# Kernel optimization log

Hardware: AMD Instinct MI355X
Metric: run time of the kernel (lower is better)

Reference implementation:

```python
import jax, jax.numpy as jnp
import numpy as np

N = 8192      # nodes; also input feature dim (x.shape[0] used as in_channels)
E = 524288    # edges per edge type (avg degree 64)
H = 200       # hidden dim (hard-coded in RecomNet)
MEAN_RATING = 3.5


def setup_inputs() -> dict:
    key = jax.random.key(0)
    ks = jax.random.split(key, 14)
    s_in = np.float32(1.0 / np.sqrt(N))
    s_h = np.float32(1.0 / np.sqrt(H))
    return {
        "x": jax.random.normal(ks[0], (N, N), jnp.float32),
        "edge_sim": jax.random.randint(ks[1], (2, E), 0, N),
        "edge_rat": jax.random.randint(ks[2], (2, E), 0, N),
        "mask": jax.random.randint(ks[3], (E,), 0, 2).astype(bool),
        # conv1 params (in=N, out=H)
        "w1_self": jax.random.normal(ks[4], (N, H), jnp.float32) * s_in,
        "w1_sim": jax.random.normal(ks[5], (N, H), jnp.float32) * s_in,
        "w1_rat": jax.random.normal(ks[6], (N, H), jnp.float32) * s_in,
        "b1": jnp.zeros((H,), jnp.float32),
        # conv2 params (in=H, out=H)
        "w2_self": jax.random.normal(ks[7], (H, H), jnp.float32) * s_h,
        "w2_sim": jax.random.normal(ks[8], (H, H), jnp.float32) * s_h,
        "w2_rat": jax.random.normal(ks[9], (H, H), jnp.float32) * s_h,
        "b2": jnp.zeros((H,), jnp.float32),
        # bilinear decoder
        "Q": jax.random.normal(ks[10], (H, H), jnp.float32) * s_h,
    }


def _recom_conv(edge_sim, edge_rat, x, w_self, w_sim, w_rat, b):
    # linear-then-gather-then-scatter (linear commutes with sum aggregation)
    m_sim = (x @ w_sim)[edge_sim[0]]                                   # [E, H]
    agg_sim = jax.ops.segment_sum(m_sim, edge_sim[1], num_segments=N)  # [N, H]
    m_rat = (x @ w_rat)[edge_rat[0]]
    agg_rat = jax.ops.segment_sum(m_rat, edge_rat[1], num_segments=N)
    return x @ w_self + agg_sim + agg_rat + b


def reference(x, w1_self, w1_sim, w1_rat, b1, w2_self, w2_sim, w2_rat, b2, Q,
              edge_sim, edge_rat, mask):
    h = _recom_conv(edge_sim, edge_rat, x, w1_self, w1_sim, w1_rat, b1)
    h = jax.nn.relu(h)
    h = _recom_conv(edge_sim, edge_rat, h, w2_self, w2_sim, w2_rat, b2)
    h1 = h[edge_rat[0]]                                                # [E, H]
    h2 = h[edge_rat[1]]                                                # [E, H]
    pred = jnp.einsum("eh,hk,ek->e", h1, Q, h2) + MEAN_RATING          # [E]
    # original compacts with boolean mask (dynamic shape); here we keep a
    # fixed [E] output and zero out unmasked edges
    return jnp.where(mask, pred, 0.0)
```

## Files before the change

kernel.cpp:

```cpp
#include <hip/hip_runtime.h>

#define NN 8192
#define EE 524288
#define HPAD 256
#define NP 640

using s16x8 = __attribute__((ext_vector_type(8))) short;
using f32x4 = __attribute__((ext_vector_type(4))) float;

__device__ __forceinline__ unsigned short f2b(float f) {
    unsigned u = __float_as_uint(f);
    u = (u + 0x7FFFu + ((u >> 16) & 1u)) >> 16;
    return (unsigned short)u;
}
__device__ __forceinline__ float b2f(unsigned short u) {
    return __uint_as_float((unsigned)u << 16);
}

__device__ __forceinline__ void async16(const unsigned short* g, unsigned short* l)
{
    __builtin_amdgcn_global_load_lds(
        (const __attribute__((address_space(1))) unsigned int*)g,
        (__attribute__((address_space(3))) unsigned int*)l, 16, 0, 0);
}


__global__ void cvt_f2b_kernel(const float* __restrict__ in,
                               unsigned short* __restrict__ out, int n4)
{
    int i = blockIdx.x * 256 + threadIdx.x;
    if (i >= n4) return;
    float4 v = ((const float4*)in)[i];
    ushort4 o;
    o.x = f2b(v.x); o.y = f2b(v.y); o.z = f2b(v.z); o.w = f2b(v.w);
    ((ushort4*)out)[i] = o;
}

__global__ void transpose_w_kernel(const float* __restrict__ w0,
                                   const float* __restrict__ w1,
                                   const float* __restrict__ w2,
                                   unsigned short* __restrict__ out,
                                   int Kout, int Kreal, int Nreal)
{
    __shared__ float tile[32][33];
    const int kb = blockIdx.x << 5;
    const int nb = blockIdx.y << 5;
    const int tx = threadIdx.x, ty = threadIdx.y;
    const int n = nb + tx;
    const float* w = (n < 200) ? w0 : (n < 400) ? w1 : w2;
    const int c = (n < 200) ? n : (n < 400) ? n - 200 : n - 400;
#pragma unroll
    for (int i = 0; i < 4; ++i) {
        const int k = kb + ty + (i << 3);
        float v = 0.f;
        if (n < Nreal && k < Kreal) v = w[(size_t)k * 200 + c];
        tile[ty + (i << 3)][tx] = v;
    }
    __syncthreads();
#pragma unroll
    for (int i = 0; i < 4; ++i) {
        const int nn = nb + ty + (i << 3);
        out[(size_t)nn * Kout + kb + tx] = f2b(tile[tx][ty + (i << 3)]);
    }
}

__global__ __launch_bounds__(256) void gemm_mfma(
    const unsigned short* __restrict__ A,
    const unsigned short* __restrict__ BT,
    float* __restrict__ C, unsigned short* __restrict__ Cb,
    int lda, int KC, int ldc, size_t planeStride)
{
    __shared__ unsigned short As[2][128 * 64];
    __shared__ unsigned short Bs[2][128 * 64];
    const int tid  = threadIdx.x;
    const int lane = tid & 63;
    const int w    = tid >> 6;

    const int nx   = gridDim.x;
    const int flat = blockIdx.y * nx + blockIdx.x;
    const int cpx  = (nx * gridDim.y) >> 3;
    const int orig = (flat & 7) * cpx + (flat >> 3);
    const int by   = orig / nx;
    const int bx   = orig - by * nx;

    const int row0 = by << 7;
    const int col0 = bx << 7;
    const int z    = blockIdx.z;
    const int wm = (w >> 1) << 6;
    const int wn = (w & 1) << 6;

    const int sr = lane >> 3;
    const int sc = (lane & 7) ^ sr;
    const size_t kbase = (size_t)z * KC + ((size_t)sc << 3);
    const unsigned short* aG = A  + (size_t)(row0 + w * 8 + sr) * lda + kbase;
    const unsigned short* bG = BT + (size_t)(col0 + w * 8 + sr) * lda + kbase;
    const int ldsOff = w * 8;

    const f32x4 zero = {0.f, 0.f, 0.f, 0.f};
    f32x4 acc[4][4];
#pragma unroll
    for (int i = 0; i < 4; ++i)
#pragma unroll
        for (int j = 0; j < 4; ++j) acc[i][j] = zero;

#pragma unroll
    for (int it = 0; it < 4; ++it) {
        async16(aG + (size_t)(it * 32) * lda, &As[0][(it * 32 + ldsOff) << 6]);
        async16(bG + (size_t)(it * 32) * lda, &Bs[0][(it * 32 + ldsOff) << 6]);
    }
    __syncthreads();

    const int T = KC >> 6;
    for (int t = 0; t < T; ++t) {
        const int cur = t & 1;
        if (t + 1 < T) {
            const int ko = (t + 1) << 6;
#pragma unroll
            for (int it = 0; it < 4; ++it) {
                async16(aG + (size_t)(it * 32) * lda + ko,
                        &As[cur ^ 1][(it * 32 + ldsOff) << 6]);
                async16(bG + (size_t)(it * 32) * lda + ko,
                        &Bs[cur ^ 1][(it * 32 + ldsOff) << 6]);
            }
        }
#pragma unroll
        for (int kk = 0; kk < 2; ++kk) {
            const int q  = (kk << 2) + (lane >> 4);
            const int sl = (q ^ (lane & 7)) << 3;
            s16x8 af[4], bfv[4];
#pragma unroll
            for (int i = 0; i < 4; ++i) {
                const int rm = wm + (i << 4) + (lane & 15);
                af[i]  = *(const s16x8*)(&As[cur][(rm << 6) + sl]);
                const int rn = wn + (i << 4) + (lane & 15);
                bfv[i] = *(const s16x8*)(&Bs[cur][(rn << 6) + sl]);
            }
#pragma unroll
            for (int i = 0; i < 4; ++i)
#pragma unroll
                for (int j = 0; j < 4; ++j)
                    acc[i][j] = __builtin_amdgcn_mfma_f32_16x16x32_bf16(
                        af[i], bfv[j], acc[i][j], 0, 0, 0);
        }
        __syncthreads();
    }

    const int cr = (lane >> 4) << 2;
    const int cc = lane & 15;
    if (Cb) {
#pragma unroll
        for (int i = 0; i < 4; ++i)
#pragma unroll
            for (int j = 0; j < 4; ++j)
#pragma unroll
                for (int r = 0; r < 4; ++r)
                    Cb[(size_t)(row0 + wm + (i << 4) + cr + r) * ldc
                       + (col0 + wn + (j << 4) + cc)] = f2b(acc[i][j][r]);
    } else {
        float* Cp = C + (size_t)z * planeStride;
#pragma unroll
        for (int i = 0; i < 4; ++i)
#pragma unroll
            for (int j = 0; j < 4; ++j)
#pragma unroll
                for (int r = 0; r < 4; ++r)
                    Cp[(size_t)(row0 + wm + (i << 4) + cr + r) * ldc
                       + (col0 + wn + (j << 4) + cc)] = acc[i][j][r];
    }
}

__global__ void combine_kernel(const float* __restrict__ p0,
                               const float* __restrict__ p1,
                               float* __restrict__ y_self,
                               unsigned short* __restrict__ y_simb,
                               unsigned short* __restrict__ y_ratb)
{
    int t = blockIdx.x * 256 + threadIdx.x;
    int n = t / 50, j4 = (t - n * 50) << 2;
    const float* a = p0 + (size_t)n * NP;
    float4 s = *(const float4*)(a + j4);
    float4 m = *(const float4*)(a + 200 + j4);
    float4 r = *(const float4*)(a + 400 + j4);
    if (p1) {
        const float* b = p1 + (size_t)n * NP;
        float4 s2 = *(const float4*)(b + j4);
        float4 m2 = *(const float4*)(b + 200 + j4);
        float4 r2 = *(const float4*)(b + 400 + j4);
        s.x += s2.x; s.y += s2.y; s.z += s2.z; s.w += s2.w;
        m.x += m2.x; m.y += m2.y; m.z += m2.z; m.w += m2.w;
        r.x += r2.x; r.y += r2.y; r.z += r2.z; r.w += r2.w;
    }
    *(float4*)(y_self + (size_t)n * 200 + j4) = s;
    ushort4 mo, ro;
    mo.x = f2b(m.x); mo.y = f2b(m.y); mo.z = f2b(m.z); mo.w = f2b(m.w);
    ro.x = f2b(r.x); ro.y = f2b(r.y); ro.z = f2b(r.z); ro.w = f2b(r.w);
    *(ushort4*)(y_simb + (size_t)n * 200 + j4) = mo;
    *(ushort4*)(y_ratb + (size_t)n * 200 + j4) = ro;
}


__global__ void hist_kernel(const int* __restrict__ e0, const int* __restrict__ e1,
                            int* __restrict__ d0, int* __restrict__ d1)
{
    const int* edges = blockIdx.y ? e1 : e0;
    int* deg = blockIdx.y ? d1 : d0;
    int e = blockIdx.x * 256 + threadIdx.x;
    if (e < EE) atomicAdd(&deg[edges[EE + e]], 1);
}

__global__ void scan_kernel(const int* __restrict__ deg0, int* __restrict__ off0,
                            int* __restrict__ pos0,
                            const int* __restrict__ deg1, int* __restrict__ off1,
                            int* __restrict__ pos1)
{
    const int* deg = blockIdx.x ? deg1 : deg0;
    int* off = blockIdx.x ? off1 : off0;
    int* pos = blockIdx.x ? pos1 : pos0;
    __shared__ int part[256];
    const int t = threadIdx.x;
    const int base = t * 32;
    int s = 0;
#pragma unroll
    for (int i = 0; i < 32; ++i) s += deg[base + i];
    part[t] = s;
    __syncthreads();
    for (int d = 1; d < 256; d <<= 1) {
        int v = (t >= d) ? part[t - d] : 0;
        __syncthreads();
        part[t] += v;
        __syncthreads();
    }
    int run = (t == 0) ? 0 : part[t - 1];
    for (int i = 0; i < 32; ++i) {
        off[base + i] = run;
        pos[base + i] = run;
        run += deg[base + i];
    }
    if (t == 255) off[NN] = run;
}

__global__ void reorder_kernel(const int* __restrict__ e0, int* __restrict__ pos0,
                               int2* __restrict__ se0,
                               const int* __restrict__ e1, int* __restrict__ pos1,
                               int2* __restrict__ se1)
{
    const int* edges = blockIdx.y ? e1 : e0;
    int* pos = blockIdx.y ? pos1 : pos0;
    int2* se = blockIdx.y ? se1 : se0;
    int e = blockIdx.x * 256 + threadIdx.x;
    if (e >= EE) return;
    int p = atomicAdd(&pos[edges[EE + e]], 1);
    se[p] = make_int2(edges[e], e);
}


__device__ __forceinline__ void edge_accum(
    const unsigned short* __restrict__ msg,
    const int* __restrict__ off, const int2* __restrict__ se,
    int n, int w, int j4, bool act, float4& acc)
{
    const int e1 = off[n + 1];
    int i = off[n] + w;
    for (; i + 12 < e1; i += 16) {
        const int s0 = se[i].x;
        const int s1 = se[i + 4].x;
        const int s2 = se[i + 8].x;
        const int s3 = se[i + 12].x;
        if (act) {
            ushort4 v0 = *(const ushort4*)(msg + (size_t)s0 * 200 + j4);
            ushort4 v1 = *(const ushort4*)(msg + (size_t)s1 * 200 + j4);
            ushort4 v2 = *(const ushort4*)(msg + (size_t)s2 * 200 + j4);
            ushort4 v3 = *(const ushort4*)(msg + (size_t)s3 * 200 + j4);
            acc.x += (b2f(v0.x) + b2f(v1.x)) + (b2f(v2.x) + b2f(v3.x));
            acc.y += (b2f(v0.y) + b2f(v1.y)) + (b2f(v2.y) + b2f(v3.y));
            acc.z += (b2f(v0.z) + b2f(v1.z)) + (b2f(v2.z) + b2f(v3.z));
            acc.w += (b2f(v0.w) + b2f(v1.w)) + (b2f(v2.w) + b2f(v3.w));
        }
    }
    for (; i < e1; i += 4) {
        const int s = se[i].x;
        if (act) {
            ushort4 v = *(const ushort4*)(msg + (size_t)s * 200 + j4);
            acc.x += b2f(v.x); acc.y += b2f(v.y);
            acc.z += b2f(v.z); acc.w += b2f(v.w);
        }
    }
}

__global__ __launch_bounds__(256) void agg_fused_kernel(
    const unsigned short* __restrict__ msg_sim,
    const unsigned short* __restrict__ msg_rat,
    const int* __restrict__ off_sim, const int2* __restrict__ se_sim,
    const int* __restrict__ off_rat, const int2* __restrict__ se_rat,
    const float* __restrict__ y_self, const float* __restrict__ bias,
    unsigned short* __restrict__ hb, int relu)
{
    __shared__ float part[4][200];
    const int n = blockIdx.x;
    const int w = threadIdx.x >> 6;
    const int lane = threadIdx.x & 63;
    const int j4 = lane << 2;
    const bool act = lane < 50;

    float4 acc = {0.f, 0.f, 0.f, 0.f};
    edge_accum(msg_sim, off_sim, se_sim, n, w, j4, act, acc);
    edge_accum(msg_rat, off_rat, se_rat, n, w, j4, act, acc);

    if (act) *(float4*)&part[w][j4] = acc;
    __syncthreads();
    const int j = threadIdx.x;
    if (j < 200) {
        float v = part[0][j] + part[1][j] + part[2][j] + part[3][j]
                + y_self[(size_t)n * 200 + j] + bias[j];
        if (relu) v = fmaxf(v, 0.f);
        hb[((size_t)n << 8) + j] = f2b(v);
    } else if (j < HPAD) {
        hb[((size_t)n << 8) + j] = 0;
    }
}

__global__ __launch_bounds__(256) void pred_kernel(
    const unsigned short* __restrict__ hQb,
    const unsigned short* __restrict__ h2b,
    const int* __restrict__ off, const int2* __restrict__ se,
    const int* __restrict__ mask, float* __restrict__ out)
{
    const int n = blockIdx.x;
    const int w = threadIdx.x >> 6;
    const int lane = threadIdx.x & 63;
    float4 b = {0.f, 0.f, 0.f, 0.f};
    if (lane < 50) {
        ushort4 v = *(const ushort4*)(h2b + ((size_t)n << 8) + (lane << 2));
        b.x = b2f(v.x); b.y = b2f(v.y); b.z = b2f(v.z); b.w = b2f(v.w);
    }
    const int e1 = off[n + 1];
    int i = off[n] + w;
    for (; i + 12 < e1; i += 16) {
        const int2 p0 = se[i];
        const int2 p1 = se[i + 4];
        const int2 p2 = se[i + 8];
        const int2 p3 = se[i + 12];
        float s0 = 0.f, s1 = 0.f, s2 = 0.f, s3 = 0.f;
        if (lane < 50) {
            ushort4 a0 = *(const ushort4*)(hQb + ((size_t)p0.x << 8) + (lane << 2));
            ushort4 a1 = *(const ushort4*)(hQb + ((size_t)p1.x << 8) + (lane << 2));
            ushort4 a2 = *(const ushort4*)(hQb + ((size_t)p2.x << 8) + (lane << 2));
            ushort4 a3 = *(const ushort4*)(hQb + ((size_t)p3.x << 8) + (lane << 2));
            s0 = fmaf(b2f(a0.x), b.x, fmaf(b2f(a0.y), b.y,
                 fmaf(b2f(a0.z), b.z, b2f(a0.w) * b.w)));
            s1 = fmaf(b2f(a1.x), b.x, fmaf(b2f(a1.y), b.y,
                 fmaf(b2f(a1.z), b.z, b2f(a1.w) * b.w)));
            s2 = fmaf(b2f(a2.x), b.x, fmaf(b2f(a2.y), b.y,
                 fmaf(b2f(a2.z), b.z, b2f(a2.w) * b.w)));
            s3 = fmaf(b2f(a3.x), b.x, fmaf(b2f(a3.y), b.y,
                 fmaf(b2f(a3.z), b.z, b2f(a3.w) * b.w)));
        }
#pragma unroll
        for (int o = 32; o > 0; o >>= 1) {
            s0 += __shfl_down(s0, o, 64);
            s1 += __shfl_down(s1, o, 64);
            s2 += __shfl_down(s2, o, 64);
            s3 += __shfl_down(s3, o, 64);
        }
        if (lane == 0) {
            out[p0.y] = mask[p0.y] ? (s0 + 3.5f) : 0.f;
            out[p1.y] = mask[p1.y] ? (s1 + 3.5f) : 0.f;
            out[p2.y] = mask[p2.y] ? (s2 + 3.5f) : 0.f;
            out[p3.y] = mask[p3.y] ? (s3 + 3.5f) : 0.f;
        }
    }
    for (; i < e1; i += 4) {
        const int2 p = se[i];
        float s = 0.f;
        if (lane < 50) {
            ushort4 a = *(const ushort4*)(hQb + ((size_t)p.x << 8) + (lane << 2));
            s = fmaf(b2f(a.x), b.x, fmaf(b2f(a.y), b.y,
                fmaf(b2f(a.z), b.z, b2f(a.w) * b.w)));
        }
#pragma unroll
        for (int o = 32; o > 0; o >>= 1) s += __shfl_down(s, o, 64);
        if (lane == 0) out[p.y] = mask[p.y] ? (s + 3.5f) : 0.f;
    }
}

extern "C" void kernel_launch(void* const* d_in, const int* in_sizes, int n_in,
                              void* d_out, int out_size, void* d_ws, size_t ws_size,
                              hipStream_t stream)
{
    const float* x       = (const float*)d_in[0];
    const int*   e_sim   = (const int*)d_in[1];
    const int*   e_rat   = (const int*)d_in[2];
    const int*   mask    = (const int*)d_in[3];
    const float* w1_self = (const float*)d_in[4];
    const float* w1_sim  = (const float*)d_in[5];
    const float* w1_rat  = (const float*)d_in[6];
    const float* b1      = (const float*)d_in[7];
    const float* w2_self = (const float*)d_in[8];
    const float* w2_sim  = (const float*)d_in[9];
    const float* w2_rat  = (const float*)d_in[10];
    const float* b2      = (const float*)d_in[11];
    const float* Q       = (const float*)d_in[12];
    float* out = (float*)d_out;

    char* p = (char*)d_ws;
    auto alloc = [&](size_t bytes) -> char* {
        char* r = p;
        p += (bytes + 255) & ~(size_t)255;
        return r;
    };
    unsigned short* xb    = (unsigned short*)alloc((size_t)NN * NN * 2);
    unsigned short* wbT1  = (unsigned short*)alloc((size_t)NP * NN * 2);
    unsigned short* wbT2  = (unsigned short*)alloc((size_t)NP * HPAD * 2);
    unsigned short* QT    = (unsigned short*)alloc((size_t)HPAD * HPAD * 2);
    float* ypart = (float*)alloc((size_t)2 * NN * NP * 4);
    float* y_self = (float*)alloc((size_t)NN * 200 * 4);
    unsigned short* y_simb = (unsigned short*)alloc((size_t)NN * 200 * 2);
    unsigned short* y_ratb = (unsigned short*)alloc((size_t)NN * 200 * 2);
    unsigned short* h1b = (unsigned short*)alloc((size_t)NN * HPAD * 2);
    unsigned short* h2b = (unsigned short*)alloc((size_t)NN * HPAD * 2);
    unsigned short* hQb = (unsigned short*)alloc((size_t)NN * HPAD * 2);
    int* deg_sim = (int*)alloc(NN * 4);
    int* deg_rat = (int*)alloc(NN * 4);
    int* off_sim = (int*)alloc((NN + 1) * 4);
    int* off_rat = (int*)alloc((NN + 1) * 4);
    int* pos_sim = (int*)alloc(NN * 4);
    int* pos_rat = (int*)alloc(NN * 4);
    int2* se_sim = (int2*)alloc((size_t)EE * 8);
    int2* se_rat = (int2*)alloc((size_t)EE * 8);

    const dim3 blk(256);
    const dim3 tblk(32, 8);

    cvt_f2b_kernel<<<(NN * NN / 4) / 256, blk, 0, stream>>>(x, xb, NN * NN / 4);
    transpose_w_kernel<<<dim3(NN / 32, NP / 32), tblk, 0, stream>>>(
        w1_self, w1_sim, w1_rat, wbT1, NN, NN, 600);
    transpose_w_kernel<<<dim3(HPAD / 32, NP / 32), tblk, 0, stream>>>(
        w2_self, w2_sim, w2_rat, wbT2, HPAD, 200, 600);
    transpose_w_kernel<<<dim3(HPAD / 32, HPAD / 32), tblk, 0, stream>>>(
        Q, Q, Q, QT, HPAD, 200, 200);

    hipMemsetAsync(deg_sim, 0, 2 * NN * 4, stream);
    hist_kernel<<<dim3(EE / 256, 2), blk, 0, stream>>>(e_sim, e_rat, deg_sim, deg_rat);
    scan_kernel<<<2, blk, 0, stream>>>(deg_sim, off_sim, pos_sim,
                                       deg_rat, off_rat, pos_rat);
    reorder_kernel<<<dim3(EE / 256, 2), blk, 0, stream>>>(
        e_sim, pos_sim, se_sim, e_rat, pos_rat, se_rat);

    gemm_mfma<<<dim3(NP / 128, NN / 128, 2), blk, 0, stream>>>(
        xb, wbT1, ypart, nullptr, NN, NN / 2, NP, (size_t)NN * NP);
    combine_kernel<<<NN * 50 / 256, blk, 0, stream>>>(
        ypart, ypart + (size_t)NN * NP, y_self, y_simb, y_ratb);
    agg_fused_kernel<<<NN, blk, 0, stream>>>(
        y_simb, y_ratb, off_sim, se_sim, off_rat, se_rat, y_self, b1, h1b, 1);

    gemm_mfma<<<dim3(NP / 128, NN / 128, 1), blk, 0, stream>>>(
        h1b, wbT2, ypart, nullptr, HPAD, HPAD, NP, 0);
    combine_kernel<<<NN * 50 / 256, blk, 0, stream>>>(
        ypart, nullptr, y_self, y_simb, y_ratb);
    agg_fused_kernel<<<NN, blk, 0, stream>>>(
        y_simb, y_ratb, off_sim, se_sim, off_rat, se_rat, y_self, b2, h2b, 0);

    gemm_mfma<<<dim3(HPAD / 128, NN / 128, 1), blk, 0, stream>>>(
        h2b, QT, nullptr, hQb, HPAD, HPAD, HPAD, 0);
    pred_kernel<<<NN, blk, 0, stream>>>(hQb, h2b, off_rat, se_rat, mask, out);
}
```

Measured before the change: 850.0 us.

## Raise layer-1 split-K to four planes and fuse layer-2 combine into GEMM epilogue

The big layer-1 GEMM (8192x640x8192) now uses split-K of 4 instead of 2, giving 1280 blocks instead of 640 so the GPU's compute units are better occupied. The combine kernel is generalized to sum an arbitrary number of partial planes. For layer 2, the GEMM epilogue now writes y_self as fp32 and y_sim/y_rat as bf16 directly, removing the intermediate fp32 buffer and one kernel launch. The cost is twice the partial-sum traffic for layer 1 and branchy, scattered epilogue stores.

```diff
diff --git a/kernel.cpp b/kernel.cpp
--- a/kernel.cpp
+++ b/kernel.cpp
@@ -68,7 +68,9 @@
     const unsigned short* __restrict__ A,
     const unsigned short* __restrict__ BT,
     float* __restrict__ C, unsigned short* __restrict__ Cb,
-    int lda, int KC, int ldc, size_t planeStride)
+    int lda, int KC, int ldc, size_t planeStride,
+    float* __restrict__ ys, unsigned short* __restrict__ ysb,
+    unsigned short* __restrict__ yrb)
 {
     __shared__ unsigned short As[2][128 * 64];
     __shared__ unsigned short Bs[2][128 * 64];
@@ -147,7 +149,21 @@
 
     const int cr = (lane >> 4) << 2;
     const int cc = lane & 15;
-    if (Cb) {
+    if (ysb) {
+#pragma unroll
+        for (int i = 0; i < 4; ++i)
+#pragma unroll
+            for (int j = 0; j < 4; ++j)
+#pragma unroll
+                for (int r = 0; r < 4; ++r) {
+                    const int n = row0 + wm + (i << 4) + cr + r;
+                    const int c = col0 + wn + (j << 4) + cc;
+                    const float v = acc[i][j][r];
+                    if (c < 200)      ys [(size_t)n * 200 + c]        = v;
+                    else if (c < 400) ysb[(size_t)n * 200 + (c - 200)] = f2b(v);
+                    else if (c < 600) yrb[(size_t)n * 200 + (c - 400)] = f2b(v);
+                }
+    } else if (Cb) {
 #pragma unroll
         for (int i = 0; i < 4; ++i)
 #pragma unroll
@@ -169,23 +185,21 @@
     }
 }
 
-__global__ void combine_kernel(const float* __restrict__ p0,
-                               const float* __restrict__ p1,
+__global__ void combine_kernel(const float* __restrict__ parts, int nplanes,
                                float* __restrict__ y_self,
                                unsigned short* __restrict__ y_simb,
                                unsigned short* __restrict__ y_ratb)
 {
     int t = blockIdx.x * 256 + threadIdx.x;
     int n = t / 50, j4 = (t - n * 50) << 2;
-    const float* a = p0 + (size_t)n * NP;
-    float4 s = *(const float4*)(a + j4);
-    float4 m = *(const float4*)(a + 200 + j4);
-    float4 r = *(const float4*)(a + 400 + j4);
-    if (p1) {
-        const float* b = p1 + (size_t)n * NP;
-        float4 s2 = *(const float4*)(b + j4);
-        float4 m2 = *(const float4*)(b + 200 + j4);
-        float4 r2 = *(const float4*)(b + 400 + j4);
+    float4 s = {0.f, 0.f, 0.f, 0.f};
+    float4 m = {0.f, 0.f, 0.f, 0.f};
+    float4 r = {0.f, 0.f, 0.f, 0.f};
+    for (int z = 0; z < nplanes; ++z) {
+        const float* a = parts + (size_t)z * NN * NP + (size_t)n * NP;
+        float4 s2 = *(const float4*)(a + j4);
+        float4 m2 = *(const float4*)(a + 200 + j4);
+        float4 r2 = *(const float4*)(a + 400 + j4);
         s.x += s2.x; s.y += s2.y; s.z += s2.z; s.w += s2.w;
         m.x += m2.x; m.y += m2.y; m.z += m2.z; m.w += m2.w;
         r.x += r2.x; r.y += r2.y; r.z += r2.z; r.w += r2.w;
@@ -412,7 +426,7 @@
     unsigned short* wbT1  = (unsigned short*)alloc((size_t)NP * NN * 2);
     unsigned short* wbT2  = (unsigned short*)alloc((size_t)NP * HPAD * 2);
     unsigned short* QT    = (unsigned short*)alloc((size_t)HPAD * HPAD * 2);
-    float* ypart = (float*)alloc((size_t)2 * NN * NP * 4);
+    float* ypart = (float*)alloc((size_t)4 * NN * NP * 4);
     float* y_self = (float*)alloc((size_t)NN * 200 * 4);
     unsigned short* y_simb = (unsigned short*)alloc((size_t)NN * 200 * 2);
     unsigned short* y_ratb = (unsigned short*)alloc((size_t)NN * 200 * 2);
@@ -446,21 +460,22 @@
     reorder_kernel<<<dim3(EE / 256, 2), blk, 0, stream>>>(
         e_sim, pos_sim, se_sim, e_rat, pos_rat, se_rat);
 
-    gemm_mfma<<<dim3(NP / 128, NN / 128, 2), blk, 0, stream>>>(
-        xb, wbT1, ypart, nullptr, NN, NN / 2, NP, (size_t)NN * NP);
+    gemm_mfma<<<dim3(NP / 128, NN / 128, 4), blk, 0, stream>>>(
+        xb, wbT1, ypart, nullptr, NN, NN / 4, NP, (size_t)NN * NP,
+        nullptr, nullptr, nullptr);
     combine_kernel<<<NN * 50 / 256, blk, 0, stream>>>(
-        ypart, ypart + (size_t)NN * NP, y_self, y_simb, y_ratb);
+        ypart, 4, y_self, y_simb, y_ratb);
     agg_fused_kernel<<<NN, blk, 0, stream>>>(
         y_simb, y_ratb, off_sim, se_sim, off_rat, se_rat, y_self, b1, h1b, 1);
 
     gemm_mfma<<<dim3(NP / 128, NN / 128, 1), blk, 0, stream>>>(
-        h1b, wbT2, ypart, nullptr, HPAD, HPAD, NP, 0);
-    combine_kernel<<<NN * 50 / 256, blk, 0, stream>>>(
-        ypart, nullptr, y_self, y_simb, y_ratb);
+        h1b, wbT2, nullptr, nullptr, HPAD, HPAD, NP, 0,
+        y_self, y_simb, y_ratb);
     agg_fused_kernel<<<NN, blk, 0, stream>>>(
         y_simb, y_ratb, off_sim, se_sim, off_rat, se_rat, y_self, b2, h2b, 0);
 
     gemm_mfma<<<dim3(HPAD / 128, NN / 128, 1), blk, 0, stream>>>(
-        h2b, QT, nullptr, hQb, HPAD, HPAD, HPAD, 0);
+        h2b, QT, nullptr, hQb, HPAD, HPAD, HPAD, 0,
+        nullptr, nullptr, nullptr);
     pred_kernel<<<NN, blk, 0, stream>>>(hQb, h2b, off_rat, se_rat, mask, out);
 }
```

Result: no change. 836.3 us (-1.6%).
